# Kernel tuning notes

Hardware: AMD Instinct MI355X
Metric: run time of the kernel (lower is better)

## Reference

```python
import jax, jax.numpy as jnp
import numpy as np

N = 50000
ALPHA = 0.1
LAMDA = 0.5


def setup_inputs() -> dict:
    key = jax.random.key(0)
    ks = jax.random.split(key, 8)
    E, IN, H, C, L = 800000, 512, 128, 40, 8
    features = jax.random.normal(ks[0], (N, IN), dtype=jnp.float32)
    edge_index = jax.random.randint(ks[1], (2, E), 0, N, dtype=jnp.int32)
    norm_A = jax.random.uniform(ks[2], (E,), dtype=jnp.float32) * 0.1
    w_fc0 = jax.random.normal(ks[3], (IN, H), dtype=jnp.float32) / np.sqrt(IN)
    b_fc0 = jnp.zeros((H,), dtype=jnp.float32)
    conv_w = jax.random.normal(ks[4], (L, H, H), dtype=jnp.float32) / np.sqrt(H)
    w_fc1 = jax.random.normal(ks[5], (H, C), dtype=jnp.float32) / np.sqrt(H)
    b_fc1 = jnp.zeros((C,), dtype=jnp.float32)
    return {"features": features, "edge_index": edge_index, "norm_A": norm_A,
            "w_fc0": w_fc0, "b_fc0": b_fc0, "conv_w": conv_w,
            "w_fc1": w_fc1, "b_fc1": b_fc1}


def _spmm(edge_index, w, x):
    # y[dst] += w_e * x[src]  over all edges; x: [N, H]
    src, dst = edge_index[0], edge_index[1]
    msgs = x[src] * w[:, None]                      # [E, H]
    return jax.ops.segment_sum(msgs, dst, num_segments=N)


def reference(features, edge_index, norm_A, w_fc0, b_fc0, conv_w, w_fc1, b_fc1):
    # dropout p=0.0 -> identity
    x = jax.nn.relu(features @ w_fc0 + b_fc0)       # [N, H]
    h0 = x
    L = conv_w.shape[0]
    for i in range(L):
        l = i + 1
        beta = jnp.log(LAMDA / l + 1.0).astype(x.dtype)
        hi = _spmm(edge_index, norm_A, x)           # Â x
        support = (1.0 - ALPHA) * hi + ALPHA * h0   # initial residual
        # identity mapping: beta * (support W) + (1-beta) * support
        x = jax.nn.relu(beta * (support @ conv_w[i]) + (1.0 - beta) * support)
    return x @ w_fc1 + b_fc1                        # [N, C]
```

## Files before the change

kernel.cpp:

```cpp
#include <hip/hip_runtime.h>
#include <hip/hip_bf16.h>
#include <math.h>

#define N_NODES 50000
#define M_PAD   50048
#define E_EDGES 800000
#define IN_DIM  512
#define HDIM    128
#define CDIM    40
#define LAYERS  8
#define NB      196

typedef __attribute__((ext_vector_type(8))) short short8;
typedef __attribute__((ext_vector_type(4))) float floatx4;
typedef unsigned short ushort_t;

__device__ inline float bf2f(unsigned short u) {
    return __uint_as_float(((unsigned)u) << 16);
}
__device__ inline unsigned short f2bf(float v) {
    __hip_bfloat16 b = __float2bfloat16(v);
    return *reinterpret_cast<unsigned short*>(&b);
}


__global__ void hist_kernel(const int* __restrict__ dst, int* __restrict__ cnt) {
    int i = blockIdx.x * blockDim.x + threadIdx.x;
    if (i < E_EDGES) atomicAdd(&cnt[dst[i]], 1);
}

__global__ void scanA(const int* __restrict__ cnt, int* __restrict__ bsum) {
    __shared__ int sm[256];
    int t = threadIdx.x, i = blockIdx.x * 256 + t;
    sm[t] = (i < N_NODES) ? cnt[i] : 0;
    __syncthreads();
    for (int d = 128; d > 0; d >>= 1) {
        if (t < d) sm[t] += sm[t + d];
        __syncthreads();
    }
    if (t == 0) bsum[blockIdx.x] = sm[0];
}

__global__ void scanB(const int* __restrict__ bsum, int* __restrict__ boff) {
    __shared__ int sm[256];
    int t = threadIdx.x;
    sm[t] = (t < NB) ? bsum[t] : 0;
    __syncthreads();
    for (int d = 1; d < 256; d <<= 1) {
        int v = (t >= d) ? sm[t - d] : 0;
        __syncthreads();
        sm[t] += v;
        __syncthreads();
    }
    if (t < NB) boff[t] = (t > 0) ? sm[t - 1] : 0;
}

__global__ void scanC(const int* __restrict__ cnt, const int* __restrict__ boff,
                      int* __restrict__ row_start, int* __restrict__ cursor) {
    __shared__ int sm[256];
    int t = threadIdx.x, i = blockIdx.x * 256 + t;
    int v = (i < N_NODES) ? cnt[i] : 0;
    sm[t] = v;
    __syncthreads();
    for (int d = 1; d < 256; d <<= 1) {
        int x = (t >= d) ? sm[t - d] : 0;
        __syncthreads();
        sm[t] += x;
        __syncthreads();
    }
    if (i < N_NODES) {
        int incl = boff[blockIdx.x] + sm[t];
        int excl = incl - v;
        row_start[i] = excl;
        cursor[i]    = excl;
        if (i == N_NODES - 1) row_start[N_NODES] = incl;
    }
}

__global__ void scatter_kernel(const int* __restrict__ ei, const float* __restrict__ normA,
                               int* __restrict__ cursor, int2* __restrict__ perm) {
    int i = blockIdx.x * blockDim.x + threadIdx.x;
    if (i >= E_EDGES) return;
    int d = ei[E_EDGES + i];
    int idx = atomicAdd(&cursor[d], 1);
    perm[idx] = make_int2(ei[i], __float_as_int(normA[i]));
}


__global__ void prep_weights(const float* __restrict__ W0, const float* __restrict__ convW,
                             const float* __restrict__ W1,
                             ushort_t* __restrict__ Wt0, ushort_t* __restrict__ WtL,
                             ushort_t* __restrict__ Wt1) {
    int i = blockIdx.x * blockDim.x + threadIdx.x;
    if (i < 128 * 512) {
        int n = i >> 9, k = i & 511;
        Wt0[i] = f2bf(W0[k * HDIM + n]);
        return;
    }
    int j = i - 128 * 512;
    if (j < 8 * 128 * 128) {
        int l = j >> 14, rem = j & 16383, n = rem >> 7, k = rem & 127;
        WtL[j] = f2bf(convW[l * 16384 + k * HDIM + n]);
        return;
    }
    int m = j - 8 * 128 * 128;
    if (m < 48 * 128) {
        int n = m >> 7, k = m & 127;
        Wt1[m] = (n < CDIM) ? f2bf(W1[k * CDIM + n]) : (ushort_t)0;
    }
}


__global__ __launch_bounds__(256)
void fc0_mfma(const float* __restrict__ F, const ushort_t* __restrict__ Wt0,
              const float* __restrict__ b0, ushort_t* __restrict__ h0b) {
    int t = threadIdx.x;
    int wave = t >> 6, lane = t & 63;
    int quad = lane >> 4, l16 = lane & 15;
    int R0 = blockIdx.x * 128 + wave * 32;

    int r0 = R0 + l16;      if (r0 > N_NODES - 1) r0 = N_NODES - 1;
    int r1 = R0 + 16 + l16; if (r1 > N_NODES - 1) r1 = N_NODES - 1;
    const float* ap0 = F + (size_t)r0 * IN_DIM + quad * 8;
    const float* ap1 = F + (size_t)r1 * IN_DIM + quad * 8;
    const ushort_t* bbase = Wt0 + (size_t)l16 * IN_DIM + quad * 8;

    floatx4 acc0[8], acc1[8];
#pragma unroll
    for (int nt = 0; nt < 8; nt++) {
        acc0[nt] = (floatx4){0.f, 0.f, 0.f, 0.f};
        acc1[nt] = (floatx4){0.f, 0.f, 0.f, 0.f};
    }

    float4 pa00 = *(const float4*)(ap0);
    float4 pa01 = *(const float4*)(ap0 + 4);
    float4 pa10 = *(const float4*)(ap1);
    float4 pa11 = *(const float4*)(ap1 + 4);
    float4 pb00 = *(const float4*)(ap0 + 32);
    float4 pb01 = *(const float4*)(ap0 + 36);
    float4 pb10 = *(const float4*)(ap1 + 32);
    float4 pb11 = *(const float4*)(ap1 + 36);

#pragma unroll
    for (int kk = 0; kk < 16; kk += 2) {
        short8 a0, a1;
        a0[0] = (short)f2bf(pa00.x); a0[1] = (short)f2bf(pa00.y);
        a0[2] = (short)f2bf(pa00.z); a0[3] = (short)f2bf(pa00.w);
        a0[4] = (short)f2bf(pa01.x); a0[5] = (short)f2bf(pa01.y);
        a0[6] = (short)f2bf(pa01.z); a0[7] = (short)f2bf(pa01.w);
        a1[0] = (short)f2bf(pa10.x); a1[1] = (short)f2bf(pa10.y);
        a1[2] = (short)f2bf(pa10.z); a1[3] = (short)f2bf(pa10.w);
        a1[4] = (short)f2bf(pa11.x); a1[5] = (short)f2bf(pa11.y);
        a1[6] = (short)f2bf(pa11.z); a1[7] = (short)f2bf(pa11.w);
        if (kk + 2 < 16) {
            pa00 = *(const float4*)(ap0 + (kk + 2) * 32);
            pa01 = *(const float4*)(ap0 + (kk + 2) * 32 + 4);
            pa10 = *(const float4*)(ap1 + (kk + 2) * 32);
            pa11 = *(const float4*)(ap1 + (kk + 2) * 32 + 4);
        }
#pragma unroll
        for (int nt = 0; nt < 8; nt++) {
            short8 b = *(const short8*)(bbase + (size_t)nt * 16 * IN_DIM + kk * 32);
            acc0[nt] = __builtin_amdgcn_mfma_f32_16x16x32_bf16(a0, b, acc0[nt], 0, 0, 0);
            acc1[nt] = __builtin_amdgcn_mfma_f32_16x16x32_bf16(a1, b, acc1[nt], 0, 0, 0);
        }
        short8 c0, c1;
        c0[0] = (short)f2bf(pb00.x); c0[1] = (short)f2bf(pb00.y);
        c0[2] = (short)f2bf(pb00.z); c0[3] = (short)f2bf(pb00.w);
        c0[4] = (short)f2bf(pb01.x); c0[5] = (short)f2bf(pb01.y);
        c0[6] = (short)f2bf(pb01.z); c0[7] = (short)f2bf(pb01.w);
        c1[0] = (short)f2bf(pb10.x); c1[1] = (short)f2bf(pb10.y);
        c1[2] = (short)f2bf(pb10.z); c1[3] = (short)f2bf(pb10.w);
        c1[4] = (short)f2bf(pb11.x); c1[5] = (short)f2bf(pb11.y);
        c1[6] = (short)f2bf(pb11.z); c1[7] = (short)f2bf(pb11.w);
        if (kk + 3 < 16) {
            pb00 = *(const float4*)(ap0 + (kk + 3) * 32);
            pb01 = *(const float4*)(ap0 + (kk + 3) * 32 + 4);
            pb10 = *(const float4*)(ap1 + (kk + 3) * 32);
            pb11 = *(const float4*)(ap1 + (kk + 3) * 32 + 4);
        }
#pragma unroll
        for (int nt = 0; nt < 8; nt++) {
            short8 b = *(const short8*)(bbase + (size_t)nt * 16 * IN_DIM + (kk + 1) * 32);
            acc0[nt] = __builtin_amdgcn_mfma_f32_16x16x32_bf16(c0, b, acc0[nt], 0, 0, 0);
            acc1[nt] = __builtin_amdgcn_mfma_f32_16x16x32_bf16(c1, b, acc1[nt], 0, 0, 0);
        }
    }

#pragma unroll
    for (int nt = 0; nt < 8; nt++) {
        int col = nt * 16 + l16;
        float bias = b0[col];
#pragma unroll
        for (int r = 0; r < 4; r++) {
            int row = R0 + quad * 4 + r;
            float v = acc0[nt][r] + bias;
            v = v > 0.f ? v : 0.f;
            h0b[(size_t)row * HDIM + col] = f2bf(v);
        }
#pragma unroll
        for (int r = 0; r < 4; r++) {
            int row = R0 + 16 + quad * 4 + r;
            float v = acc1[nt][r] + bias;
            v = v > 0.f ? v : 0.f;
            h0b[(size_t)row * HDIM + col] = f2bf(v);
        }
    }
}


#define SROW 136

__global__ __launch_bounds__(256)
void layer_fused(const int* __restrict__ row_start, const int2* __restrict__ perm,
                 const ushort_t* __restrict__ xb, const ushort_t* __restrict__ h0b,
                 const ushort_t* __restrict__ Wt, ushort_t* __restrict__ X,
                 float beta) {
    __shared__ short sS[64][SROW];
    int t = threadIdx.x;
    int wave = t >> 6, lane = t & 63;
    int grp = lane >> 4, sl = lane & 15;
    int quad = lane >> 4, l16 = lane & 15;
    int row0 = blockIdx.x * 64;
    int G = wave * 4 + grp;
    int Rg = row0 + G * 4;

    for (int r = 0; r < 4; r++) {
        int row = Rg + r;
        int i0 = row < N_NODES ? row : N_NODES;
        int i1 = row + 1 < N_NODES ? row + 1 : N_NODES;
        int e0 = row_start[i0];
        int e1 = row_start[i1];

        float acc[8];
#pragma unroll
        for (int c = 0; c < 8; c++) acc[c] = 0.f;

        for (int chunk = e0; chunk < e1; chunk += 16) {
            int2 pm = make_int2(0, 0);
            if (chunk + sl < e1) pm = perm[chunk + sl];
#pragma unroll
            for (int d = 0; d < 16; d += 4) {
                int   s0 = __shfl(pm.x, d + 0, 16);
                int   s1 = __shfl(pm.x, d + 1, 16);
                int   s2 = __shfl(pm.x, d + 2, 16);
                int   s3 = __shfl(pm.x, d + 3, 16);
                float w0 = __int_as_float(__shfl(pm.y, d + 0, 16));
                float w1 = __int_as_float(__shfl(pm.y, d + 1, 16));
                float w2 = __int_as_float(__shfl(pm.y, d + 2, 16));
                float w3 = __int_as_float(__shfl(pm.y, d + 3, 16));
                short8 v0 = *(const short8*)(xb + (size_t)s0 * HDIM + sl * 8);
                short8 v1 = *(const short8*)(xb + (size_t)s1 * HDIM + sl * 8);
                short8 v2 = *(const short8*)(xb + (size_t)s2 * HDIM + sl * 8);
                short8 v3 = *(const short8*)(xb + (size_t)s3 * HDIM + sl * 8);
#pragma unroll
                for (int c = 0; c < 8; c++) {
                    acc[c] += w0 * bf2f((ushort_t)v0[c]);
                    acc[c] += w1 * bf2f((ushort_t)v1[c]);
                    acc[c] += w2 * bf2f((ushort_t)v2[c]);
                    acc[c] += w3 * bf2f((ushort_t)v3[c]);
                }
            }
        }

        short8 o;
        if (row < N_NODES) {
            short8 h = *(const short8*)(h0b + (size_t)row * HDIM + sl * 8);
#pragma unroll
            for (int c = 0; c < 8; c++)
                o[c] = (short)f2bf(0.9f * acc[c] + 0.1f * bf2f((ushort_t)h[c]));
        } else {
#pragma unroll
            for (int c = 0; c < 8; c++) o[c] = 0;
        }
        *(short8*)&sS[G * 4 + r][sl * 8] = o;
    }
    __syncthreads();

    short8 afrag[4];
#pragma unroll
    for (int ks = 0; ks < 4; ks++)
        afrag[ks] = *(const short8*)&sS[wave * 16 + l16][ks * 32 + quad * 8];

    floatx4 gacc[8];
#pragma unroll
    for (int nt = 0; nt < 8; nt++) {
        const ushort_t* bp = Wt + (size_t)(nt * 16 + l16) * HDIM + quad * 8;
        floatx4 c = (floatx4){0.f, 0.f, 0.f, 0.f};
#pragma unroll
        for (int ks = 0; ks < 4; ks++) {
            short8 b = *(const short8*)(bp + ks * 32);
            c = __builtin_amdgcn_mfma_f32_16x16x32_bf16(afrag[ks], b, c, 0, 0, 0);
        }
        gacc[nt] = c;
    }
    float g = 1.f - beta;
#pragma unroll
    for (int nt = 0; nt < 8; nt++) {
        int col = nt * 16 + l16;
#pragma unroll
        for (int r = 0; r < 4; r++) {
            int lrow = wave * 16 + quad * 4 + r;
            float s = bf2f((ushort_t)sS[lrow][col]);
            float v = beta * gacc[nt][r] + g * s;
            v = v > 0.f ? v : 0.f;
            X[(size_t)(row0 + lrow) * HDIM + col] = f2bf(v);
        }
    }
}


__global__ void fc1_mfma(const ushort_t* __restrict__ X, const ushort_t* __restrict__ Wt1,
                         const float* __restrict__ b1, float* __restrict__ out) {
    int wave = threadIdx.x >> 6;
    int lane = threadIdx.x & 63;
    int quad = lane >> 4, l16 = lane & 15;
    int row0 = blockIdx.x * 64 + wave * 16;

    int arow = row0 + l16; if (arow > N_NODES - 1) arow = N_NODES - 1;
    const ushort_t* ap = X + (size_t)arow * HDIM + quad * 8;
    short8 afrag[4];
#pragma unroll
    for (int ks = 0; ks < 4; ks++) afrag[ks] = *(const short8*)(ap + ks * 32);

    floatx4 acc[3];
#pragma unroll
    for (int nt = 0; nt < 3; nt++) {
        const ushort_t* bp = Wt1 + (size_t)(nt * 16 + l16) * HDIM + quad * 8;
        floatx4 c = (floatx4){0.f, 0.f, 0.f, 0.f};
#pragma unroll
        for (int ks = 0; ks < 4; ks++) {
            short8 b = *(const short8*)(bp + ks * 32);
            c = __builtin_amdgcn_mfma_f32_16x16x32_bf16(afrag[ks], b, c, 0, 0, 0);
        }
        acc[nt] = c;
    }
#pragma unroll
    for (int nt = 0; nt < 3; nt++) {
        int col = nt * 16 + l16;
        if (col < CDIM) {
            float bias = b1[col];
#pragma unroll
            for (int r = 0; r < 4; r++) {
                int row = row0 + quad * 4 + r;
                if (row < N_NODES)
                    out[(size_t)row * CDIM + col] = acc[nt][r] + bias;
            }
        }
    }
}


extern "C" void kernel_launch(void* const* d_in, const int* in_sizes, int n_in,
                              void* d_out, int out_size, void* d_ws, size_t ws_size,
                              hipStream_t stream) {
    const float* F     = (const float*)d_in[0];
    const int*   ei    = (const int*)d_in[1];
    const float* normA = (const float*)d_in[2];
    const float* W0    = (const float*)d_in[3];
    const float* b0    = (const float*)d_in[4];
    const float* convW = (const float*)d_in[5];
    const float* W1    = (const float*)d_in[6];
    const float* b1    = (const float*)d_in[7];
    float*       out   = (float*)d_out;

    ushort_t* h0b  = (ushort_t*)d_ws;
    ushort_t* xab  = h0b + (size_t)M_PAD * HDIM;
    ushort_t* xbb  = xab + (size_t)M_PAD * HDIM;
    ushort_t* Wt0  = xbb + (size_t)M_PAD * HDIM;
    ushort_t* WtL  = Wt0 + 128 * 512;
    ushort_t* Wt1  = WtL + 8 * 128 * 128;
    int*   row_start = (int*)(Wt1 + 48 * 128);
    int*   cursor    = row_start + (N_NODES + 8);
    int*   cnt       = cursor + (N_NODES + 8);
    int*   bsum      = cnt + (N_NODES + 8);
    int*   boff      = bsum + 256;
    int2*  perm      = (int2*)(boff + 256);

    hipMemsetAsync(cnt, 0, N_NODES * sizeof(int), stream);
    hist_kernel<<<(E_EDGES + 255) / 256, 256, 0, stream>>>(ei + E_EDGES, cnt);
    scanA<<<NB, 256, 0, stream>>>(cnt, bsum);
    scanB<<<1, 256, 0, stream>>>(bsum, boff);
    scanC<<<NB, 256, 0, stream>>>(cnt, boff, row_start, cursor);
    scatter_kernel<<<(E_EDGES + 255) / 256, 256, 0, stream>>>(ei, normA, cursor, perm);
    prep_weights<<<(128 * 512 + 8 * 128 * 128 + 48 * 128 + 255) / 256, 256, 0, stream>>>(
        W0, convW, W1, Wt0, WtL, Wt1);

    fc0_mfma<<<M_PAD / 128, 256, 0, stream>>>(F, Wt0, b0, h0b);

    ushort_t* ping = h0b;
    ushort_t* pong = xab;
    for (int i = 0; i < LAYERS; i++) {
        float beta = logf(0.5f / (float)(i + 1) + 1.0f);
        layer_fused<<<M_PAD / 64, 256, 0, stream>>>(
            row_start, perm, ping, h0b, WtL + (size_t)i * HDIM * HDIM, pong, beta);
        if (i == 0) { ping = xab; pong = xbb; }
        else { ushort_t* tmp = ping; ping = pong; pong = tmp; }
    }
    fc1_mfma<<<M_PAD / 64, 256, 0, stream>>>(ping, Wt1, b1, out);
}
```

Baseline: 732.1 us.

## Deepen fc0 prefetch and batch SpMM edge loads across four rows

In fc0, all eight k-steps of features are preloaded into registers and refilled eight steps ahead instead of two, and the launch bound now requests one block per CU so the compiler may use more registers. In the fused layer kernel, each 16-lane group reads its four row_start offsets with one load and a shuffle. It then fetches the first 32 edges for all four rows up front and processes edges 32 at a time, so more gathers are in flight at once. This targets memory latency in the feature stream and the irregular gather, at the cost of higher register pressure and possibly lower occupancy.

Result: slower. 1.320 ms (+80.4%).

```diff
diff --git a/kernel.cpp b/kernel.cpp
--- a/kernel.cpp
+++ b/kernel.cpp
@@ -111,7 +111,7 @@
 }
 
 
-__global__ __launch_bounds__(256)
+__global__ __launch_bounds__(256, 1)
 void fc0_mfma(const float* __restrict__ F, const ushort_t* __restrict__ Wt0,
               const float* __restrict__ b0, ushort_t* __restrict__ h0b) {
     int t = threadIdx.x;
@@ -132,58 +132,39 @@
         acc1[nt] = (floatx4){0.f, 0.f, 0.f, 0.f};
     }
 
-    float4 pa00 = *(const float4*)(ap0);
-    float4 pa01 = *(const float4*)(ap0 + 4);
-    float4 pa10 = *(const float4*)(ap1);
-    float4 pa11 = *(const float4*)(ap1 + 4);
-    float4 pb00 = *(const float4*)(ap0 + 32);
-    float4 pb01 = *(const float4*)(ap0 + 36);
-    float4 pb10 = *(const float4*)(ap1 + 32);
-    float4 pb11 = *(const float4*)(ap1 + 36);
-
-#pragma unroll
-    for (int kk = 0; kk < 16; kk += 2) {
+    float4 pf[8][4];
+#pragma unroll
+    for (int d = 0; d < 8; d++) {
+        pf[d][0] = *(const float4*)(ap0 + d * 32);
+        pf[d][1] = *(const float4*)(ap0 + d * 32 + 4);
+        pf[d][2] = *(const float4*)(ap1 + d * 32);
+        pf[d][3] = *(const float4*)(ap1 + d * 32 + 4);
+    }
+
+#pragma unroll
+    for (int ks = 0; ks < 16; ks++) {
+        float4 lo0 = pf[ks & 7][0], hi0 = pf[ks & 7][1];
+        float4 lo1 = pf[ks & 7][2], hi1 = pf[ks & 7][3];
         short8 a0, a1;
-        a0[0] = (short)f2bf(pa00.x); a0[1] = (short)f2bf(pa00.y);
-        a0[2] = (short)f2bf(pa00.z); a0[3] = (short)f2bf(pa00.w);
-        a0[4] = (short)f2bf(pa01.x); a0[5] = (short)f2bf(pa01.y);
-        a0[6] = (short)f2bf(pa01.z); a0[7] = (short)f2bf(pa01.w);
-        a1[0] = (short)f2bf(pa10.x); a1[1] = (short)f2bf(pa10.y);
-        a1[2] = (short)f2bf(pa10.z); a1[3] = (short)f2bf(pa10.w);
-        a1[4] = (short)f2bf(pa11.x); a1[5] = (short)f2bf(pa11.y);
-        a1[6] = (short)f2bf(pa11.z); a1[7] = (short)f2bf(pa11.w);
-        if (kk + 2 < 16) {
-            pa00 = *(const float4*)(ap0 + (kk + 2) * 32);
-            pa01 = *(const float4*)(ap0 + (kk + 2) * 32 + 4);
-            pa10 = *(const float4*)(ap1 + (kk + 2) * 32);
-            pa11 = *(const float4*)(ap1 + (kk + 2) * 32 + 4);
+        a0[0] = (short)f2bf(lo0.x); a0[1] = (short)f2bf(lo0.y);
+        a0[2] = (short)f2bf(lo0.z); a0[3] = (short)f2bf(lo0.w);
+        a0[4] = (short)f2bf(hi0.x); a0[5] = (short)f2bf(hi0.y);
+        a0[6] = (short)f2bf(hi0.z); a0[7] = (short)f2bf(hi0.w);
+        a1[0] = (short)f2bf(lo1.x); a1[1] = (short)f2bf(lo1.y);
+        a1[2] = (short)f2bf(lo1.z); a1[3] = (short)f2bf(lo1.w);
+        a1[4] = (short)f2bf(hi1.x); a1[5] = (short)f2bf(hi1.y);
+        a1[6] = (short)f2bf(hi1.z); a1[7] = (short)f2bf(hi1.w);
+        if (ks + 8 < 16) {
+            pf[ks & 7][0] = *(const float4*)(ap0 + (ks + 8) * 32);
+            pf[ks & 7][1] = *(const float4*)(ap0 + (ks + 8) * 32 + 4);
+            pf[ks & 7][2] = *(const float4*)(ap1 + (ks + 8) * 32);
+            pf[ks & 7][3] = *(const float4*)(ap1 + (ks + 8) * 32 + 4);
         }
 #pragma unroll
         for (int nt = 0; nt < 8; nt++) {
-            short8 b = *(const short8*)(bbase + (size_t)nt * 16 * IN_DIM + kk * 32);
+            short8 b = *(const short8*)(bbase + (size_t)nt * 16 * IN_DIM + ks * 32);
             acc0[nt] = __builtin_amdgcn_mfma_f32_16x16x32_bf16(a0, b, acc0[nt], 0, 0, 0);
             acc1[nt] = __builtin_amdgcn_mfma_f32_16x16x32_bf16(a1, b, acc1[nt], 0, 0, 0);
-        }
-        short8 c0, c1;
-        c0[0] = (short)f2bf(pb00.x); c0[1] = (short)f2bf(pb00.y);
-        c0[2] = (short)f2bf(pb00.z); c0[3] = (short)f2bf(pb00.w);
-        c0[4] = (short)f2bf(pb01.x); c0[5] = (short)f2bf(pb01.y);
-        c0[6] = (short)f2bf(pb01.z); c0[7] = (short)f2bf(pb01.w);
-        c1[0] = (short)f2bf(pb10.x); c1[1] = (short)f2bf(pb10.y);
-        c1[2] = (short)f2bf(pb10.z); c1[3] = (short)f2bf(pb10.w);
-        c1[4] = (short)f2bf(pb11.x); c1[5] = (short)f2bf(pb11.y);
-        c1[6] = (short)f2bf(pb11.z); c1[7] = (short)f2bf(pb11.w);
-        if (kk + 3 < 16) {
-            pb00 = *(const float4*)(ap0 + (kk + 3) * 32);
-            pb01 = *(const float4*)(ap0 + (kk + 3) * 32 + 4);
-            pb10 = *(const float4*)(ap1 + (kk + 3) * 32);
-            pb11 = *(const float4*)(ap1 + (kk + 3) * 32 + 4);
-        }
-#pragma unroll
-        for (int nt = 0; nt < 8; nt++) {
-            short8 b = *(const short8*)(bbase + (size_t)nt * 16 * IN_DIM + (kk + 1) * 32);
-            acc0[nt] = __builtin_amdgcn_mfma_f32_16x16x32_bf16(c0, b, acc0[nt], 0, 0, 0);
-            acc1[nt] = __builtin_amdgcn_mfma_f32_16x16x32_bf16(c1, b, acc1[nt], 0, 0, 0);
         }
     }
 
@@ -210,6 +191,32 @@
 
 
 #define SROW 136
+
+__device__ __forceinline__ void spmm_proc16(int2 pm, const ushort_t* __restrict__ xb,
+                                            int sl, float* __restrict__ acc) {
+#pragma unroll
+    for (int j = 0; j < 16; j += 4) {
+        int   s0 = __shfl(pm.x, j + 0, 16);
+        int   s1 = __shfl(pm.x, j + 1, 16);
+        int   s2 = __shfl(pm.x, j + 2, 16);
+        int   s3 = __shfl(pm.x, j + 3, 16);
+        float w0 = __int_as_float(__shfl(pm.y, j + 0, 16));
+        float w1 = __int_as_float(__shfl(pm.y, j + 1, 16));
+        float w2 = __int_as_float(__shfl(pm.y, j + 2, 16));
+        float w3 = __int_as_float(__shfl(pm.y, j + 3, 16));
+        short8 v0 = *(const short8*)(xb + (size_t)s0 * HDIM + sl * 8);
+        short8 v1 = *(const short8*)(xb + (size_t)s1 * HDIM + sl * 8);
+        short8 v2 = *(const short8*)(xb + (size_t)s2 * HDIM + sl * 8);
+        short8 v3 = *(const short8*)(xb + (size_t)s3 * HDIM + sl * 8);
+#pragma unroll
+        for (int c = 0; c < 8; c++) {
+            acc[c] += w0 * bf2f((ushort_t)v0[c]);
+            acc[c] += w1 * bf2f((ushort_t)v1[c]);
+            acc[c] += w2 * bf2f((ushort_t)v2[c]);
+            acc[c] += w3 * bf2f((ushort_t)v3[c]);
+        }
+    }
+}
 
 __global__ __launch_bounds__(256)
 void layer_fused(const int* __restrict__ row_start, const int2* __restrict__ perm,
@@ -225,50 +232,60 @@
     int G = wave * 4 + grp;
     int Rg = row0 + G * 4;
 
+    int rbv = 0;
+    if (sl <= 4) {
+        int idx = Rg + sl; if (idx > N_NODES) idx = N_NODES;
+        rbv = row_start[idx];
+    }
+    int e0[4], e1[4];
+#pragma unroll
+    for (int r = 0; r < 4; r++) {
+        e0[r] = __shfl(rbv, r, 16);
+        e1[r] = __shfl(rbv, r + 1, 16);
+    }
+
+    float acc[4][8];
+#pragma unroll
+    for (int r = 0; r < 4; r++)
+#pragma unroll
+        for (int c = 0; c < 8; c++) acc[r][c] = 0.f;
+
+    int2 pmA[4], pmB[4];
+#pragma unroll
+    for (int r = 0; r < 4; r++) {
+        pmA[r] = make_int2(0, 0);
+        pmB[r] = make_int2(0, 0);
+        int ea = e0[r] + sl;
+        int eb = e0[r] + 16 + sl;
+        if (ea < e1[r]) pmA[r] = perm[ea];
+        if (eb < e1[r]) pmB[r] = perm[eb];
+    }
+#pragma unroll
+    for (int r = 0; r < 4; r++) {
+        spmm_proc16(pmA[r], xb, sl, acc[r]);
+        spmm_proc16(pmB[r], xb, sl, acc[r]);
+    }
+#pragma unroll
+    for (int r = 0; r < 4; r++) {
+        for (int chunk = e0[r] + 32; chunk < e1[r]; chunk += 32) {
+            int2 qa = make_int2(0, 0), qb = make_int2(0, 0);
+            int ea = chunk + sl, eb = chunk + 16 + sl;
+            if (ea < e1[r]) qa = perm[ea];
+            if (eb < e1[r]) qb = perm[eb];
+            spmm_proc16(qa, xb, sl, acc[r]);
+            spmm_proc16(qb, xb, sl, acc[r]);
+        }
+    }
+
+#pragma unroll
     for (int r = 0; r < 4; r++) {
         int row = Rg + r;
-        int i0 = row < N_NODES ? row : N_NODES;
-        int i1 = row + 1 < N_NODES ? row + 1 : N_NODES;
-        int e0 = row_start[i0];
-        int e1 = row_start[i1];
-
-        float acc[8];
-#pragma unroll
-        for (int c = 0; c < 8; c++) acc[c] = 0.f;
-
-        for (int chunk = e0; chunk < e1; chunk += 16) {
-            int2 pm = make_int2(0, 0);
-            if (chunk + sl < e1) pm = perm[chunk + sl];
-#pragma unroll
-            for (int d = 0; d < 16; d += 4) {
-                int   s0 = __shfl(pm.x, d + 0, 16);
-                int   s1 = __shfl(pm.x, d + 1, 16);
-                int   s2 = __shfl(pm.x, d + 2, 16);
-                int   s3 = __shfl(pm.x, d + 3, 16);
-                float w0 = __int_as_float(__shfl(pm.y, d + 0, 16));
-                float w1 = __int_as_float(__shfl(pm.y, d + 1, 16));
-                float w2 = __int_as_float(__shfl(pm.y, d + 2, 16));
-                float w3 = __int_as_float(__shfl(pm.y, d + 3, 16));
-                short8 v0 = *(const short8*)(xb + (size_t)s0 * HDIM + sl * 8);
-                short8 v1 = *(const short8*)(xb + (size_t)s1 * HDIM + sl * 8);
-                short8 v2 = *(const short8*)(xb + (size_t)s2 * HDIM + sl * 8);
-                short8 v3 = *(const short8*)(xb + (size_t)s3 * HDIM + sl * 8);
-#pragma unroll
-                for (int c = 0; c < 8; c++) {
-                    acc[c] += w0 * bf2f((ushort_t)v0[c]);
-                    acc[c] += w1 * bf2f((ushort_t)v1[c]);
-                    acc[c] += w2 * bf2f((ushort_t)v2[c]);
-                    acc[c] += w3 * bf2f((ushort_t)v3[c]);
-                }
-            }
-        }
-
         short8 o;
         if (row < N_NODES) {
             short8 h = *(const short8*)(h0b + (size_t)row * HDIM + sl * 8);
 #pragma unroll
             for (int c = 0; c < 8; c++)
-                o[c] = (short)f2bf(0.9f * acc[c] + 0.1f * bf2f((ushort_t)h[c]));
+                o[c] = (short)f2bf(0.9f * acc[r][c] + 0.1f * bf2f((ushort_t)h[c]));
         } else {
 #pragma unroll
             for (int c = 0; c < 8; c++) o[c] = 0;
```
